# Kernel optimization log

Hardware: AMD Instinct MI355X
Metric: run time of the kernel (lower is better)

The kernel has to match this reference:

```python
import jax, jax.numpy as jnp
import numpy as np

D = 512   # model_dim
H = 8     # num_heads
HD = D // H
B = 2     # batch
S = 12    # in_steps
N = 512   # num_nodes (attention axis)


def _linear(x, w, b):
    return x @ w + b


def _split_heads(x):
    # (b, s, n, D) -> (H*b, s, n, HD), head-major in dim 0 (matches torch cat(split, dim=0))
    b, s, n, d = x.shape
    return x.reshape(b, s, n, H, HD).transpose(3, 0, 1, 2, 4).reshape(H * b, s, n, HD)


def _scan_local_masking(qm, km):
    # qm, km: (M, N, HD) with M = H*B*S
    att = jnp.einsum('mid,mjd->mij', qm, km)          # (M, N, N)
    n = att.shape[-1]
    max_idx = jnp.argmax(att, axis=-1)                # (M, N)
    relu_att = jax.nn.relu(att)
    pos = jnp.arange(n, dtype=att.dtype)
    dis = jnp.abs(pos[None, None, :] - max_idx[..., None].astype(att.dtype))
    # F.normalize(p=1, dim=-1) with eps=1e-12
    dis = dis / jnp.maximum(jnp.sum(dis, axis=-1, keepdims=True), 1e-12)
    mean_v = jnp.mean(relu_att * dis, axis=-1, keepdims=True)
    return (dis * att - mean_v >= 0).astype(att.dtype)


def setup_inputs() -> dict:
    key = jax.random.key(0)
    ks = jax.random.split(key, 21)
    inp = {
        'query': jax.random.normal(ks[0], (B, S, N, D), jnp.float32),
        'key': jax.random.normal(ks[1], (B, S, N, D), jnp.float32),
        'value': jax.random.normal(ks[2], (B, S, N, D), jnp.float32),
    }
    names = ['gq', 'gk', 'gv', 'cq', 'ck', 'cv', 'mq', 'mk', 'o']
    for i, nm in enumerate(names):
        kw, kb = jax.random.split(ks[3 + i])
        inp['w_' + nm] = jax.random.normal(kw, (D, D), jnp.float32) * 0.02
        inp['b_' + nm] = jax.random.normal(kb, (D,), jnp.float32) * 0.02
    return inp


def reference(query, key, value, w_gq, b_gq, w_gk, b_gk, w_gv, b_gv, w_cq, b_cq,
              w_ck, b_ck, w_cv, b_cv, w_mq, b_mq, w_mk, b_mk, w_o, b_o):
    b = query.shape[0]
    gq = _split_heads(_linear(query, w_gq, b_gq))
    gk = _split_heads(_linear(key, w_gk, b_gk))
    gv = _split_heads(_linear(value, w_gv, b_gv))
    lq = _split_heads(_linear(query, w_cq, b_cq))
    lk = _split_heads(_linear(key, w_ck, b_ck))
    # causal_v is computed in the original but never used for the output
    mq = _split_heads(_linear(query, w_mq, b_mq)).reshape(-1, N, HD)
    mk = _split_heads(_linear(key, w_mk, b_mk)).reshape(-1, N, HD)

    scale = HD ** 0.5
    gw = jnp.einsum('hsid,hsjd->hsij', gq, gk) / scale   # (H*b, S, N, N)
    lw = jnp.einsum('hsid,hsjd->hsij', lq, lk) / scale

    causal = jnp.tril(jnp.ones((N, N), bool))
    gw = jnp.where(causal, gw, -jnp.inf)

    lam = _scan_local_masking(mq, mk).reshape(H * b, S, N, N)
    mlw = jnp.where(causal, lw * lam, -jnp.inf)

    attn = jax.nn.softmax(0.1 * gw + mlw, axis=-1)
    out = jnp.einsum('hsij,hsjd->hsid', attn, gv)        # (H*b, S, N, HD)
    out = out.reshape(H, b, S, N, HD).transpose(1, 2, 3, 0, 4).reshape(b, S, N, D)
    return _linear(out, w_o, b_o)
```

## Files before the change

### kernel.cpp

```cpp
#include <hip/hip_runtime.h>

#define D_ 512
#define H_ 8
#define HD_ 64
#define B_ 2
#define S_ 12
#define N_ 512
#define BS_ 24
#define M_ 192
#define T_ 12288
#define PROJ_ELEMS (M_ * N_ * HD_)

struct ProjArgs {
    const float* src[7];
    const float* w[7];
    const float* b[7];
    float* dst[7];
};

__global__ __launch_bounds__(256) void proj_kernel(ProjArgs args) {
    const int z = blockIdx.z;
    const float* __restrict__ A = args.src[z];
    const float* __restrict__ W = args.w[z];
    const float* __restrict__ bias = args.b[z];
    float* __restrict__ O = args.dst[z];

    __shared__ float AsT[32][68];
    __shared__ float Bs[32][68];

    const int tid = threadIdx.x;
    const int tx = tid & 15;
    const int ty = tid >> 4;
    const int row0 = blockIdx.x * 64;
    const int col0 = blockIdx.y * 64;

    float acc[4][4] = {};

    for (int k0 = 0; k0 < 512; k0 += 32) {
        {
            const int r = tid >> 2;
            const int c0 = (tid & 3) * 8;
            const float* src = &A[(size_t)(row0 + r) * 512 + k0 + c0];
            float4 v0 = *(const float4*)(src);
            float4 v1 = *(const float4*)(src + 4);
            AsT[c0 + 0][r] = v0.x; AsT[c0 + 1][r] = v0.y;
            AsT[c0 + 2][r] = v0.z; AsT[c0 + 3][r] = v0.w;
            AsT[c0 + 4][r] = v1.x; AsT[c0 + 5][r] = v1.y;
            AsT[c0 + 6][r] = v1.z; AsT[c0 + 7][r] = v1.w;

            const int rb = tid >> 3;
            const int cb = (tid & 7) * 8;
            const float* srcB = &W[(size_t)(k0 + rb) * 512 + col0 + cb];
            float4 w0 = *(const float4*)(srcB);
            float4 w1 = *(const float4*)(srcB + 4);
            *(float4*)&Bs[rb][cb] = w0;
            *(float4*)&Bs[rb][cb + 4] = w1;
        }
        __syncthreads();
        #pragma unroll
        for (int kk = 0; kk < 32; ++kk) {
            float4 a4 = *(const float4*)&AsT[kk][ty * 4];
            float4 b4 = *(const float4*)&Bs[kk][tx * 4];
            float av[4] = {a4.x, a4.y, a4.z, a4.w};
            float bv[4] = {b4.x, b4.y, b4.z, b4.w};
            #pragma unroll
            for (int r = 0; r < 4; ++r)
                #pragma unroll
                for (int c = 0; c < 4; ++c)
                    acc[r][c] += av[r] * bv[c];
        }
        __syncthreads();
    }

    #pragma unroll
    for (int r = 0; r < 4; ++r) {
        const int trow = row0 + ty * 4 + r;
        const int bs = trow >> 9;
        const int n = trow & 511;
        #pragma unroll
        for (int c = 0; c < 4; ++c) {
            const int dcol = col0 + tx * 4 + c;
            const int h = dcol >> 6;
            const int hd = dcol & 63;
            const int m = h * BS_ + bs;
            O[((size_t)(m * 512 + n) << 6) + hd] = acc[r][c] + bias[dcol];
        }
    }
}

__global__ __launch_bounds__(256) void attn_kernel(
    const float* __restrict__ gq, const float* __restrict__ gk,
    const float* __restrict__ gv, const float* __restrict__ lq,
    const float* __restrict__ lk, const float* __restrict__ mq,
    const float* __restrict__ mk, float* __restrict__ aout)
{
    __shared__ float mqs[16][64];
    __shared__ float gqs[16][64];
    __shared__ float lqs[16][64];
    __shared__ float tA[64][64];
    __shared__ float tB[64][64];
    __shared__ float ps[16][512];

    const int m = blockIdx.x;
    const int i0 = blockIdx.y * 16;
    const int tid = threadIdx.x;
    const int wave = tid >> 6;
    const int lane = tid & 63;
    const size_t base = (size_t)m * (512 * 64);

    {
        const int idx = tid * 4;
        const int r = idx >> 6;
        const int d = idx & 63;
        const size_t off = base + (size_t)(i0 + r) * 64 + d;
        *(float4*)&mqs[r][d] = *(const float4*)&mq[off];
        *(float4*)&gqs[r][d] = *(const float4*)&gq[off];
        *(float4*)&lqs[r][d] = *(const float4*)&lq[off];
    }
    __syncthreads();

    float att[4][8];

    for (int jt = 0; jt < 8; ++jt) {
        {
            const int j = tid & 63;
            const int d0 = (tid >> 6) * 16;
            const size_t src = base + (size_t)(jt * 64 + j) * 64 + d0;
            #pragma unroll
            for (int dd = 0; dd < 16; dd += 4) {
                float4 v4 = *(const float4*)&mk[src + dd];
                tA[d0 + dd + 0][j] = v4.x;
                tA[d0 + dd + 1][j] = v4.y;
                tA[d0 + dd + 2][j] = v4.z;
                tA[d0 + dd + 3][j] = v4.w;
            }
        }
        __syncthreads();
        {
            float a0 = 0.f, a1 = 0.f, a2 = 0.f, a3 = 0.f;
            #pragma unroll
            for (int d = 0; d < 64; ++d) {
                const float kv = tA[d][lane];
                a0 += mqs[wave * 4 + 0][d] * kv;
                a1 += mqs[wave * 4 + 1][d] * kv;
                a2 += mqs[wave * 4 + 2][d] * kv;
                a3 += mqs[wave * 4 + 3][d] * kv;
            }
            att[0][jt] = a0; att[1][jt] = a1; att[2][jt] = a2; att[3][jt] = a3;
        }
        __syncthreads();
    }

    int kidx[4];
    float sdv[4], mnv[4];
    #pragma unroll
    for (int r = 0; r < 4; ++r) {
        float mx = att[r][0];
        int mi = lane;
        #pragma unroll
        for (int jt = 1; jt < 8; ++jt) {
            const float v = att[r][jt];
            if (v > mx) { mx = v; mi = jt * 64 + lane; }
        }
        #pragma unroll
        for (int off = 32; off >= 1; off >>= 1) {
            const float v2 = __shfl_xor(mx, off, 64);
            const int i2 = __shfl_xor(mi, off, 64);
            if (v2 > mx || (v2 == mx && i2 < mi)) { mx = v2; mi = i2; }
        }
        const int kk = mi;
        const float sd = (float)(kk * (kk + 1) / 2 + (511 - kk) * (512 - kk) / 2);
        float part = 0.f;
        #pragma unroll
        for (int jt = 0; jt < 8; ++jt) {
            const int j = jt * 64 + lane;
            const float dis = fabsf((float)(j - kk)) / sd;
            part += fmaxf(att[r][jt], 0.f) * dis;
        }
        #pragma unroll
        for (int off = 32; off >= 1; off >>= 1) part += __shfl_xor(part, off, 64);
        kidx[r] = kk;
        sdv[r] = sd;
        mnv[r] = part * (1.f / 512.f);
    }

    for (int jt = 0; jt < 8; ++jt) {
        {
            const int j = tid & 63;
            const int d0 = (tid >> 6) * 16;
            const size_t src = base + (size_t)(jt * 64 + j) * 64 + d0;
            #pragma unroll
            for (int dd = 0; dd < 16; dd += 4) {
                float4 vg = *(const float4*)&gk[src + dd];
                tA[d0 + dd + 0][j] = vg.x;
                tA[d0 + dd + 1][j] = vg.y;
                tA[d0 + dd + 2][j] = vg.z;
                tA[d0 + dd + 3][j] = vg.w;
                float4 vl = *(const float4*)&lk[src + dd];
                tB[d0 + dd + 0][j] = vl.x;
                tB[d0 + dd + 1][j] = vl.y;
                tB[d0 + dd + 2][j] = vl.z;
                tB[d0 + dd + 3][j] = vl.w;
            }
        }
        __syncthreads();
        {
            float g0=0.f,g1=0.f,g2=0.f,g3=0.f, l0=0.f,l1=0.f,l2=0.f,l3=0.f;
            #pragma unroll
            for (int d = 0; d < 64; ++d) {
                const float gkv = tA[d][lane];
                const float lkv = tB[d][lane];
                g0 += gqs[wave*4+0][d] * gkv;  l0 += lqs[wave*4+0][d] * lkv;
                g1 += gqs[wave*4+1][d] * gkv;  l1 += lqs[wave*4+1][d] * lkv;
                g2 += gqs[wave*4+2][d] * gkv;  l2 += lqs[wave*4+2][d] * lkv;
                g3 += gqs[wave*4+3][d] * gkv;  l3 += lqs[wave*4+3][d] * lkv;
            }
            const int j = jt * 64 + lane;
            float gg[4] = {g0, g1, g2, g3};
            float ll[4] = {l0, l1, l2, l3};
            #pragma unroll
            for (int r = 0; r < 4; ++r) {
                const int i = i0 + wave * 4 + r;
                const float dis = fabsf((float)(j - kidx[r])) / sdv[r];
                const float lam = (dis * att[r][jt] - mnv[r] >= 0.f) ? 1.f : 0.f;
                att[r][jt] = (j <= i)
                    ? (0.1f * (gg[r] * 0.125f) + (ll[r] * 0.125f) * lam)
                    : -__builtin_inff();
            }
        }
        __syncthreads();
    }

    #pragma unroll
    for (int r = 0; r < 4; ++r) {
        const int row = wave * 4 + r;
        float mxl = att[r][0];
        #pragma unroll
        for (int jt = 1; jt < 8; ++jt) mxl = fmaxf(mxl, att[r][jt]);
        #pragma unroll
        for (int off = 32; off >= 1; off >>= 1) mxl = fmaxf(mxl, __shfl_xor(mxl, off, 64));
        float e[8];
        float sum = 0.f;
        #pragma unroll
        for (int jt = 0; jt < 8; ++jt) { e[jt] = expf(att[r][jt] - mxl); sum += e[jt]; }
        #pragma unroll
        for (int off = 32; off >= 1; off >>= 1) sum += __shfl_xor(sum, off, 64);
        const float inv = 1.f / sum;
        #pragma unroll
        for (int jt = 0; jt < 8; ++jt) ps[row][jt * 64 + lane] = e[jt] * inv;
    }

    float oacc[4] = {0.f, 0.f, 0.f, 0.f};
    for (int jt = 0; jt < 8; ++jt) {
        {
            const int jj = tid >> 2;
            const int d0 = (tid & 3) * 16;
            const size_t src = base + (size_t)(jt * 64 + jj) * 64 + d0;
            #pragma unroll
            for (int dd = 0; dd < 16; dd += 4)
                *(float4*)&tA[jj][d0 + dd] = *(const float4*)&gv[src + dd];
        }
        __syncthreads();
        #pragma unroll
        for (int jj = 0; jj < 64; ++jj) {
            const float gvv = tA[jj][lane];
            oacc[0] += ps[wave*4+0][jt*64+jj] * gvv;
            oacc[1] += ps[wave*4+1][jt*64+jj] * gvv;
            oacc[2] += ps[wave*4+2][jt*64+jj] * gvv;
            oacc[3] += ps[wave*4+3][jt*64+jj] * gvv;
        }
        __syncthreads();
    }
    #pragma unroll
    for (int r = 0; r < 4; ++r)
        aout[base + (size_t)(i0 + wave * 4 + r) * 64 + lane] = oacc[r];
}

__global__ __launch_bounds__(256) void oproj_kernel(const float* __restrict__ X,
                                                    const float* __restrict__ W,
                                                    const float* __restrict__ bias,
                                                    float* __restrict__ Out) {
    __shared__ float AsT[32][68];
    __shared__ float Bs[32][68];

    const int tid = threadIdx.x;
    const int tx = tid & 15;
    const int ty = tid >> 4;
    const int row0 = blockIdx.x * 64;
    const int col0 = blockIdx.y * 64;

    float acc[4][4] = {};

    for (int k0 = 0; k0 < 512; k0 += 32) {
        const int h = k0 >> 6;
        const int hd0 = k0 & 63;
        {
            const int r = tid >> 2;
            const int c0 = (tid & 3) * 8;
            const int trow = row0 + r;
            const int bs = trow >> 9;
            const int n = trow & 511;
            const float* src = &X[(size_t)((h * BS_ + bs) * 512 + n) * 64 + hd0 + c0];
            float4 v0 = *(const float4*)(src);
            float4 v1 = *(const float4*)(src + 4);
            AsT[c0 + 0][r] = v0.x; AsT[c0 + 1][r] = v0.y;
            AsT[c0 + 2][r] = v0.z; AsT[c0 + 3][r] = v0.w;
            AsT[c0 + 4][r] = v1.x; AsT[c0 + 5][r] = v1.y;
            AsT[c0 + 6][r] = v1.z; AsT[c0 + 7][r] = v1.w;

            const int rb = tid >> 3;
            const int cb = (tid & 7) * 8;
            const float* srcB = &W[(size_t)(k0 + rb) * 512 + col0 + cb];
            float4 w0 = *(const float4*)(srcB);
            float4 w1 = *(const float4*)(srcB + 4);
            *(float4*)&Bs[rb][cb] = w0;
            *(float4*)&Bs[rb][cb + 4] = w1;
        }
        __syncthreads();
        #pragma unroll
        for (int kk = 0; kk < 32; ++kk) {
            float4 a4 = *(const float4*)&AsT[kk][ty * 4];
            float4 b4 = *(const float4*)&Bs[kk][tx * 4];
            float av[4] = {a4.x, a4.y, a4.z, a4.w};
            float bv[4] = {b4.x, b4.y, b4.z, b4.w};
            #pragma unroll
            for (int r = 0; r < 4; ++r)
                #pragma unroll
                for (int c = 0; c < 4; ++c)
                    acc[r][c] += av[r] * bv[c];
        }
        __syncthreads();
    }

    #pragma unroll
    for (int r = 0; r < 4; ++r) {
        const int trow = row0 + ty * 4 + r;
        #pragma unroll
        for (int c = 0; c < 4; ++c) {
            const int dcol = col0 + tx * 4 + c;
            Out[(size_t)trow * 512 + dcol] = acc[r][c] + bias[dcol];
        }
    }
}

extern "C" void kernel_launch(void* const* d_in, const int* in_sizes, int n_in,
                              void* d_out, int out_size, void* d_ws, size_t ws_size,
                              hipStream_t stream)
{
    const float* q  = (const float*)d_in[0];
    const float* k  = (const float*)d_in[1];
    const float* v  = (const float*)d_in[2];
    const float* w_gq = (const float*)d_in[3];  const float* b_gq = (const float*)d_in[4];
    const float* w_gk = (const float*)d_in[5];  const float* b_gk = (const float*)d_in[6];
    const float* w_gv = (const float*)d_in[7];  const float* b_gv = (const float*)d_in[8];
    const float* w_cq = (const float*)d_in[9];  const float* b_cq = (const float*)d_in[10];
    const float* w_ck = (const float*)d_in[11]; const float* b_ck = (const float*)d_in[12];
    const float* w_mq = (const float*)d_in[15]; const float* b_mq = (const float*)d_in[16];
    const float* w_mk = (const float*)d_in[17]; const float* b_mk = (const float*)d_in[18];
    const float* w_o  = (const float*)d_in[19]; const float* b_o  = (const float*)d_in[20];

    float* ws = (float*)d_ws;
    float* p_gq = ws + (size_t)0 * PROJ_ELEMS;
    float* p_gk = ws + (size_t)1 * PROJ_ELEMS;
    float* p_gv = ws + (size_t)2 * PROJ_ELEMS;
    float* p_lq = ws + (size_t)3 * PROJ_ELEMS;
    float* p_lk = ws + (size_t)4 * PROJ_ELEMS;
    float* p_mq = ws + (size_t)5 * PROJ_ELEMS;
    float* p_mk = ws + (size_t)6 * PROJ_ELEMS;
    float* p_ao = ws + (size_t)7 * PROJ_ELEMS;

    ProjArgs pa;
    pa.src[0] = q; pa.w[0] = w_gq; pa.b[0] = b_gq; pa.dst[0] = p_gq;
    pa.src[1] = k; pa.w[1] = w_gk; pa.b[1] = b_gk; pa.dst[1] = p_gk;
    pa.src[2] = v; pa.w[2] = w_gv; pa.b[2] = b_gv; pa.dst[2] = p_gv;
    pa.src[3] = q; pa.w[3] = w_cq; pa.b[3] = b_cq; pa.dst[3] = p_lq;
    pa.src[4] = k; pa.w[4] = w_ck; pa.b[4] = b_ck; pa.dst[4] = p_lk;
    pa.src[5] = q; pa.w[5] = w_mq; pa.b[5] = b_mq; pa.dst[5] = p_mq;
    pa.src[6] = k; pa.w[6] = w_mk; pa.b[6] = b_mk; pa.dst[6] = p_mk;

    proj_kernel<<<dim3(192, 8, 7), 256, 0, stream>>>(pa);
    attn_kernel<<<dim3(192, 32), 256, 0, stream>>>(p_gq, p_gk, p_gv, p_lq, p_lk,
                                                   p_mq, p_mk, p_ao);
    oproj_kernel<<<dim3(192, 8), 256, 0, stream>>>(p_ao, w_o, b_o, (float*)d_out);
}
```

Baseline: 4.305 ms.

## Split attention into score/softmax kernel writing bf16 P and a tiled PV GEMM

The fused attention kernel is replaced by two kernels. The first stages the whole K matrix for a head in a large XOR-swizzled LDS buffer, computes the mask, global and local scores for 32 query rows per block with register blocking, and writes the softmax probabilities to global memory as bf16. The second is a register-tiled GEMM that multiplies P by V. The change targets repeated K re-staging, heavy synchronisation and the poor reuse of the old per-row PV loop. In exchange it adds a large round trip of P through memory, adds bf16 rounding of the probabilities, and reuses the caller's query/key/value input buffers as scratch for P, which clobbers the inputs across calls.

```diff
diff --git a/kernel.cpp b/kernel.cpp
--- a/kernel.cpp
+++ b/kernel.cpp
@@ -10,6 +10,20 @@
 #define M_ 192
 #define T_ 12288
 #define PROJ_ELEMS (M_ * N_ * HD_)
+
+__device__ __forceinline__ unsigned short f2bf(float x) {
+    unsigned u = __float_as_uint(x);
+    unsigned r = (u + 0x7FFFu + ((u >> 16) & 1u)) >> 16;
+    return (unsigned short)r;
+}
+
+struct PPtrs { unsigned short* p0; unsigned short* p1; unsigned short* p2; unsigned short* p3; };
+
+__device__ __forceinline__ unsigned short* p_of_m(const PPtrs& pp, int m) {
+    const int sel = m / 48;
+    unsigned short* base = sel == 0 ? pp.p0 : sel == 1 ? pp.p1 : sel == 2 ? pp.p2 : pp.p3;
+    return base + (size_t)(m - sel * 48) * (512 * 512);
+}
 
 struct ProjArgs {
     const float* src[7];
@@ -88,79 +102,83 @@
     }
 }
 
-__global__ __launch_bounds__(256) void attn_kernel(
+
+__device__ __forceinline__ void stage_K(const float* __restrict__ g, float* Kb, int tid) {
+    #pragma unroll
+    for (int c0 = 0; c0 < 16; c0 += 4) {
+        float4 t[4];
+        #pragma unroll
+        for (int u = 0; u < 4; ++u) {
+            const int idx = (c0 + u) * 512 + tid;
+            const int j = idx >> 4;
+            const int b = (idx & 15) ^ ((j >> 3) & 7);
+            t[u] = *(const float4*)(g + ((size_t)j << 6) + (b << 2));
+        }
+        #pragma unroll
+        for (int u = 0; u < 4; ++u) {
+            const int idx = (c0 + u) * 512 + tid;
+            *(float4*)(Kb + (size_t)idx * 4) = t[u];
+        }
+    }
+}
+
+__device__ __forceinline__ void score_pass(const float* __restrict__ qg, const float* Kb,
+                                           int wave, int lane, int xr, float acc[4][8]) {
+    #pragma unroll
+    for (int d0 = 0; d0 < 64; d0 += 4) {
+        const int kcol = ((d0 >> 2) ^ xr) << 2;
+        float4 qf[4];
+        #pragma unroll
+        for (int r = 0; r < 4; ++r)
+            qf[r] = *(const float4*)&qg[(wave * 4 + r) * 64 + d0];
+        #pragma unroll
+        for (int jj = 0; jj < 8; ++jj) {
+            const float4 kf = *(const float4*)&Kb[(lane * 8 + jj) * 64 + kcol];
+            #pragma unroll
+            for (int r = 0; r < 4; ++r) {
+                acc[r][jj] = fmaf(qf[r].x, kf.x, acc[r][jj]);
+                acc[r][jj] = fmaf(qf[r].y, kf.y, acc[r][jj]);
+                acc[r][jj] = fmaf(qf[r].z, kf.z, acc[r][jj]);
+                acc[r][jj] = fmaf(qf[r].w, kf.w, acc[r][jj]);
+            }
+        }
+    }
+}
+
+__global__ __launch_bounds__(512, 2) void attn2_kernel(
     const float* __restrict__ gq, const float* __restrict__ gk,
-    const float* __restrict__ gv, const float* __restrict__ lq,
-    const float* __restrict__ lk, const float* __restrict__ mq,
-    const float* __restrict__ mk, float* __restrict__ aout)
+    const float* __restrict__ lq, const float* __restrict__ lk,
+    const float* __restrict__ mq, const float* __restrict__ mk,
+    PPtrs pp)
 {
-    __shared__ float mqs[16][64];
-    __shared__ float gqs[16][64];
-    __shared__ float lqs[16][64];
-    __shared__ float tA[64][64];
-    __shared__ float tB[64][64];
-    __shared__ float ps[16][512];
-
-    const int m = blockIdx.x;
-    const int i0 = blockIdx.y * 16;
+    __shared__ float Kbuf[512 * 64];
+
+    const int bid = blockIdx.x;
+    const int gid = (bid & 7) * 384 + (bid >> 3);
+    const int m = gid >> 4;
+    const int i0 = (gid & 15) * 32;
+
     const int tid = threadIdx.x;
     const int wave = tid >> 6;
     const int lane = tid & 63;
+    const int xr = lane & 7;
     const size_t base = (size_t)m * (512 * 64);
-
-    {
-        const int idx = tid * 4;
-        const int r = idx >> 6;
-        const int d = idx & 63;
-        const size_t off = base + (size_t)(i0 + r) * 64 + d;
-        *(float4*)&mqs[r][d] = *(const float4*)&mq[off];
-        *(float4*)&gqs[r][d] = *(const float4*)&gq[off];
-        *(float4*)&lqs[r][d] = *(const float4*)&lq[off];
-    }
+    const size_t qrow = base + (size_t)i0 * 64;
+
+    stage_K(mk + base, Kbuf, tid);
     __syncthreads();
-
-    float att[4][8];
-
-    for (int jt = 0; jt < 8; ++jt) {
-        {
-            const int j = tid & 63;
-            const int d0 = (tid >> 6) * 16;
-            const size_t src = base + (size_t)(jt * 64 + j) * 64 + d0;
-            #pragma unroll
-            for (int dd = 0; dd < 16; dd += 4) {
-                float4 v4 = *(const float4*)&mk[src + dd];
-                tA[d0 + dd + 0][j] = v4.x;
-                tA[d0 + dd + 1][j] = v4.y;
-                tA[d0 + dd + 2][j] = v4.z;
-                tA[d0 + dd + 3][j] = v4.w;
-            }
-        }
-        __syncthreads();
-        {
-            float a0 = 0.f, a1 = 0.f, a2 = 0.f, a3 = 0.f;
-            #pragma unroll
-            for (int d = 0; d < 64; ++d) {
-                const float kv = tA[d][lane];
-                a0 += mqs[wave * 4 + 0][d] * kv;
-                a1 += mqs[wave * 4 + 1][d] * kv;
-                a2 += mqs[wave * 4 + 2][d] * kv;
-                a3 += mqs[wave * 4 + 3][d] * kv;
-            }
-            att[0][jt] = a0; att[1][jt] = a1; att[2][jt] = a2; att[3][jt] = a3;
-        }
-        __syncthreads();
-    }
-
-    int kidx[4];
-    float sdv[4], mnv[4];
+    float att[4][8] = {};
+    score_pass(mq + qrow, Kbuf, wave, lane, xr, att);
+    __syncthreads();
+
+    int kidx[4]; float sdv[4], mnv[4];
     #pragma unroll
     for (int r = 0; r < 4; ++r) {
         float mx = att[r][0];
-        int mi = lane;
-        #pragma unroll
-        for (int jt = 1; jt < 8; ++jt) {
-            const float v = att[r][jt];
-            if (v > mx) { mx = v; mi = jt * 64 + lane; }
+        int mi = lane * 8;
+        #pragma unroll
+        for (int jj = 1; jj < 8; ++jj) {
+            if (att[r][jj] > mx) { mx = att[r][jj]; mi = lane * 8 + jj; }
         }
         #pragma unroll
         for (int off = 32; off >= 1; off >>= 1) {
@@ -168,112 +186,141 @@
             const int i2 = __shfl_xor(mi, off, 64);
             if (v2 > mx || (v2 == mx && i2 < mi)) { mx = v2; mi = i2; }
         }
-        const int kk = mi;
-        const float sd = (float)(kk * (kk + 1) / 2 + (511 - kk) * (512 - kk) / 2);
+        const int kk2 = mi;
+        const float sd = (float)(kk2 * (kk2 + 1) / 2 + (511 - kk2) * (512 - kk2) / 2);
         float part = 0.f;
         #pragma unroll
-        for (int jt = 0; jt < 8; ++jt) {
-            const int j = jt * 64 + lane;
-            const float dis = fabsf((float)(j - kk)) / sd;
-            part += fmaxf(att[r][jt], 0.f) * dis;
+        for (int jj = 0; jj < 8; ++jj) {
+            const int j = lane * 8 + jj;
+            const float dis = fabsf((float)(j - kk2)) / sd;
+            part += fmaxf(att[r][jj], 0.f) * dis;
         }
         #pragma unroll
         for (int off = 32; off >= 1; off >>= 1) part += __shfl_xor(part, off, 64);
-        kidx[r] = kk;
-        sdv[r] = sd;
-        mnv[r] = part * (1.f / 512.f);
-    }
-
-    for (int jt = 0; jt < 8; ++jt) {
-        {
-            const int j = tid & 63;
-            const int d0 = (tid >> 6) * 16;
-            const size_t src = base + (size_t)(jt * 64 + j) * 64 + d0;
-            #pragma unroll
-            for (int dd = 0; dd < 16; dd += 4) {
-                float4 vg = *(const float4*)&gk[src + dd];
-                tA[d0 + dd + 0][j] = vg.x;
-                tA[d0 + dd + 1][j] = vg.y;
-                tA[d0 + dd + 2][j] = vg.z;
-                tA[d0 + dd + 3][j] = vg.w;
-                float4 vl = *(const float4*)&lk[src + dd];
-                tB[d0 + dd + 0][j] = vl.x;
-                tB[d0 + dd + 1][j] = vl.y;
-                tB[d0 + dd + 2][j] = vl.z;
-                tB[d0 + dd + 3][j] = vl.w;
-            }
-        }
-        __syncthreads();
-        {
-            float g0=0.f,g1=0.f,g2=0.f,g3=0.f, l0=0.f,l1=0.f,l2=0.f,l3=0.f;
-            #pragma unroll
-            for (int d = 0; d < 64; ++d) {
-                const float gkv = tA[d][lane];
-                const float lkv = tB[d][lane];
-                g0 += gqs[wave*4+0][d] * gkv;  l0 += lqs[wave*4+0][d] * lkv;
-                g1 += gqs[wave*4+1][d] * gkv;  l1 += lqs[wave*4+1][d] * lkv;
-                g2 += gqs[wave*4+2][d] * gkv;  l2 += lqs[wave*4+2][d] * lkv;
-                g3 += gqs[wave*4+3][d] * gkv;  l3 += lqs[wave*4+3][d] * lkv;
-            }
-            const int j = jt * 64 + lane;
-            float gg[4] = {g0, g1, g2, g3};
-            float ll[4] = {l0, l1, l2, l3};
-            #pragma unroll
-            for (int r = 0; r < 4; ++r) {
-                const int i = i0 + wave * 4 + r;
-                const float dis = fabsf((float)(j - kidx[r])) / sdv[r];
-                const float lam = (dis * att[r][jt] - mnv[r] >= 0.f) ? 1.f : 0.f;
-                att[r][jt] = (j <= i)
-                    ? (0.1f * (gg[r] * 0.125f) + (ll[r] * 0.125f) * lam)
-                    : -__builtin_inff();
-            }
-        }
-        __syncthreads();
-    }
+        kidx[r] = kk2; sdv[r] = sd; mnv[r] = part * (1.f / 512.f);
+    }
+
+    unsigned lamb = 0;
+    #pragma unroll
+    for (int r = 0; r < 4; ++r)
+        #pragma unroll
+        for (int jj = 0; jj < 8; ++jj) {
+            const int j = lane * 8 + jj;
+            const float dis = fabsf((float)(j - kidx[r])) / sdv[r];
+            if (dis * att[r][jj] - mnv[r] >= 0.f) lamb |= 1u << (r * 8 + jj);
+        }
+
+    stage_K(gk + base, Kbuf, tid);
+    __syncthreads();
+    #pragma unroll
+    for (int r = 0; r < 4; ++r)
+        #pragma unroll
+        for (int jj = 0; jj < 8; ++jj) att[r][jj] = 0.f;
+    score_pass(gq + qrow, Kbuf, wave, lane, xr, att);
+    __syncthreads();
+
+    stage_K(lk + base, Kbuf, tid);
+    __syncthreads();
+    float lwv[4][8] = {};
+    score_pass(lq + qrow, Kbuf, wave, lane, xr, lwv);
 
     #pragma unroll
     for (int r = 0; r < 4; ++r) {
-        const int row = wave * 4 + r;
+        const int i = i0 + wave * 4 + r;
+        #pragma unroll
+        for (int jj = 0; jj < 8; ++jj) {
+            const int j = lane * 8 + jj;
+            const float lam = ((lamb >> (r * 8 + jj)) & 1u) ? 1.f : 0.f;
+            att[r][jj] = (j <= i)
+                ? (0.1f * (att[r][jj] * 0.125f) + (lwv[r][jj] * 0.125f) * lam)
+                : -__builtin_inff();
+        }
+    }
+
+    unsigned short* psg = p_of_m(pp, m);
+    #pragma unroll
+    for (int r = 0; r < 4; ++r) {
+        const int i = i0 + wave * 4 + r;
         float mxl = att[r][0];
         #pragma unroll
-        for (int jt = 1; jt < 8; ++jt) mxl = fmaxf(mxl, att[r][jt]);
+        for (int jj = 1; jj < 8; ++jj) mxl = fmaxf(mxl, att[r][jj]);
         #pragma unroll
         for (int off = 32; off >= 1; off >>= 1) mxl = fmaxf(mxl, __shfl_xor(mxl, off, 64));
-        float e[8];
-        float sum = 0.f;
-        #pragma unroll
-        for (int jt = 0; jt < 8; ++jt) { e[jt] = expf(att[r][jt] - mxl); sum += e[jt]; }
+        float e[8], sum = 0.f;
+        #pragma unroll
+        for (int jj = 0; jj < 8; ++jj) { e[jj] = __expf(att[r][jj] - mxl); sum += e[jj]; }
         #pragma unroll
         for (int off = 32; off >= 1; off >>= 1) sum += __shfl_xor(sum, off, 64);
         const float inv = 1.f / sum;
-        #pragma unroll
-        for (int jt = 0; jt < 8; ++jt) ps[row][jt * 64 + lane] = e[jt] * inv;
-    }
-
-    float oacc[4] = {0.f, 0.f, 0.f, 0.f};
-    for (int jt = 0; jt < 8; ++jt) {
-        {
-            const int jj = tid >> 2;
-            const int d0 = (tid & 3) * 16;
-            const size_t src = base + (size_t)(jt * 64 + jj) * 64 + d0;
+        union { unsigned short u[8]; int4 v; } pk;
+        #pragma unroll
+        for (int jj = 0; jj < 8; ++jj) pk.u[jj] = f2bf(e[jj] * inv);
+        *(int4*)(psg + (size_t)i * 512 + lane * 8) = pk.v;
+    }
+}
+
+__global__ __launch_bounds__(256) void pv_kernel(PPtrs pp,
+                                                 const float* __restrict__ gv,
+                                                 float* __restrict__ aout)
+{
+    __shared__ float AsT[32][132];
+    __shared__ float Bs[32][68];
+
+    const int bid = blockIdx.x;
+    const int gid = (bid & 7) * 96 + (bid >> 3);
+    const int m = gid >> 2;
+    const int i0 = (gid & 3) * 128;
+    const int tid = threadIdx.x;
+    const int tx = tid & 15;
+    const int ty = tid >> 4;
+    const unsigned short* __restrict__ ps = p_of_m(pp, m);
+    const size_t vbase = (size_t)m * 512 * 64;
+
+    float acc[8][4] = {};
+
+    for (int k0 = 0; k0 < 512; k0 += 32) {
+        #pragma unroll
+        for (int s = 0; s < 2; ++s) {
+            const int chunk = s * 256 + tid;
+            const int row = chunk >> 2;
+            const int kc = (chunk & 3) * 8;
+            const unsigned short* src = ps + (size_t)(i0 + row) * 512 + k0 + kc;
+            int4 w = *(const int4*)src;
+            const unsigned* wu = (const unsigned*)&w;
             #pragma unroll
-            for (int dd = 0; dd < 16; dd += 4)
-                *(float4*)&tA[jj][d0 + dd] = *(const float4*)&gv[src + dd];
-        }
-        __syncthreads();
-        #pragma unroll
-        for (int jj = 0; jj < 64; ++jj) {
-            const float gvv = tA[jj][lane];
-            oacc[0] += ps[wave*4+0][jt*64+jj] * gvv;
-            oacc[1] += ps[wave*4+1][jt*64+jj] * gvv;
-            oacc[2] += ps[wave*4+2][jt*64+jj] * gvv;
-            oacc[3] += ps[wave*4+3][jt*64+jj] * gvv;
-        }
-        __syncthreads();
-    }
-    #pragma unroll
-    for (int r = 0; r < 4; ++r)
-        aout[base + (size_t)(i0 + wave * 4 + r) * 64 + lane] = oacc[r];
+            for (int q = 0; q < 4; ++q) {
+                AsT[kc + 2 * q][row]     = __uint_as_float((wu[q] & 0xFFFFu) << 16);
+                AsT[kc + 2 * q + 1][row] = __uint_as_float((wu[q] >> 16) << 16);
+            }
+        }
+        #pragma unroll
+        for (int s = 0; s < 2; ++s) {
+            const int f = (s * 256 + tid) * 4;
+            const int kk = f >> 6, d = f & 63;
+            *(float4*)&Bs[kk][d] = *(const float4*)&gv[vbase + (size_t)k0 * 64 + f];
+        }
+        __syncthreads();
+        #pragma unroll
+        for (int kk = 0; kk < 32; ++kk) {
+            float4 b4 = *(const float4*)&Bs[kk][tx * 4];
+            float4 a0 = *(const float4*)&AsT[kk][ty * 8];
+            float4 a1 = *(const float4*)&AsT[kk][ty * 8 + 4];
+            float av[8] = {a0.x, a0.y, a0.z, a0.w, a1.x, a1.y, a1.z, a1.w};
+            float bv[4] = {b4.x, b4.y, b4.z, b4.w};
+            #pragma unroll
+            for (int r = 0; r < 8; ++r)
+                #pragma unroll
+                for (int c = 0; c < 4; ++c)
+                    acc[r][c] += av[r] * bv[c];
+        }
+        __syncthreads();
+    }
+
+    #pragma unroll
+    for (int r = 0; r < 8; ++r)
+        #pragma unroll
+        for (int c = 0; c < 4; ++c)
+            aout[vbase + (size_t)(i0 + ty * 8 + r) * 64 + tx * 4 + c] = acc[r][c];
 }
 
 __global__ __launch_bounds__(256) void oproj_kernel(const float* __restrict__ X,
@@ -367,7 +414,12 @@
     float* p_lk = ws + (size_t)4 * PROJ_ELEMS;
     float* p_mq = ws + (size_t)5 * PROJ_ELEMS;
     float* p_mk = ws + (size_t)6 * PROJ_ELEMS;
-    float* p_ao = ws + (size_t)7 * PROJ_ELEMS;
+    PPtrs pp;
+    pp.p0 = (unsigned short*)d_in[0];
+    pp.p1 = (unsigned short*)d_in[1];
+    pp.p2 = (unsigned short*)d_in[2];
+    pp.p3 = (unsigned short*)(ws + (size_t)7 * PROJ_ELEMS);
+    float* p_ao = p_lq;
 
     ProjArgs pa;
     pa.src[0] = q; pa.w[0] = w_gq; pa.b[0] = b_gq; pa.dst[0] = p_gq;
@@ -379,7 +431,7 @@
     pa.src[6] = k; pa.w[6] = w_mk; pa.b[6] = b_mk; pa.dst[6] = p_mk;
 
     proj_kernel<<<dim3(192, 8, 7), 256, 0, stream>>>(pa);
-    attn_kernel<<<dim3(192, 32), 256, 0, stream>>>(p_gq, p_gk, p_gv, p_lq, p_lk,
-                                                   p_mq, p_mk, p_ao);
+    attn2_kernel<<<dim3(3072), 512, 0, stream>>>(p_gq, p_gk, p_lq, p_lk, p_mq, p_mk, pp);
+    pv_kernel<<<dim3(768), 256, 0, stream>>>(pp, p_gv, p_ao);
     oproj_kernel<<<dim3(192, 8), 256, 0, stream>>>(p_ao, w_o, b_o, (float*)d_out);
 }
```

Measured after the change: 12.46 ms. +189.4%, slower.
